# Performance work log

Measured on AMD Instinct MI355X. Metric: run time of the kernel, lower is better.

Reference implementation:

```python
import math
import jax, jax.numpy as jnp
import numpy as np

B, T, C = 2, 2048, 1024
H = 16
HD = C // H
WIN = 33
HALF = WIN // 2
CAUSAL = True
RADIUS, OMEGA, KSPR, STEP = 6.0, 1.0, 1.0, 0.1
EPS = 1e-8


def _spiral_step(x):
    # x: (..., 3) — the stacked (q, k, v) axis; D=3 -> rotate (x0, x1) pair.
    r = jnp.maximum(jnp.linalg.norm(x, axis=-1, keepdims=True), EPS)
    radial = (RADIUS - r) * (x / r)
    c = jnp.float32(math.cos(OMEGA * STEP))
    s = jnp.float32(math.sin(OMEGA * STEP))
    xi, xj, xl = x[..., 0], x[..., 1], x[..., 2]
    y = jnp.stack([c * xi - s * xj, s * xi + c * xj, xl], axis=-1)
    return x + STEP * (y - x + KSPR * radial)


def setup_inputs() -> dict:
    key = jax.random.key(0)
    ks = jax.random.split(key, 3)
    x = jax.random.normal(ks[0], (B, T, C), dtype=jnp.float32)
    W_attn = jax.random.normal(ks[1], (C, 3 * C), dtype=jnp.float32) * (1.0 / math.sqrt(C))
    W_proj = jax.random.normal(ks[2], (C, C), dtype=jnp.float32) * (1.0 / math.sqrt(C))
    sinks = jnp.zeros((H,), dtype=jnp.float32)
    ln_scale = jnp.ones((1,), dtype=jnp.float32) * 0.9
    ln_delta = jnp.ones((C,), dtype=jnp.float32)
    ln_bias = jnp.zeros((C,), dtype=jnp.float32)
    return {"x": x, "W_attn": W_attn, "W_proj": W_proj, "sinks": sinks,
            "ln_scale": ln_scale, "ln_delta": ln_delta, "ln_bias": ln_bias}


def reference(x, W_attn, W_proj, sinks, ln_scale, ln_delta, ln_bias):
    qkv = x @ W_attn                              # (B,T,3C)
    q, k, v = jnp.split(qkv, 3, axis=-1)          # each (B,T,C)

    # SpiralMix over the stacked (q,k,v) axis, loop_iters=2. Only q,k are
    # taken from the mixed output (v stays the pre-spiral value), matching src.
    s = jnp.stack([q, k, v], axis=-1)             # (B,T,C,3)
    s = _spiral_step(_spiral_step(s))
    q, k = s[..., 0], s[..., 1]

    def to_heads(t):
        return t.reshape(B, T, H, HD).transpose(0, 2, 1, 3)  # (B,H,T,hd)
    q, k, v = to_heads(q), to_heads(k), to_heads(v)

    # local window index
    t_idx = jnp.arange(T)
    offs = jnp.arange(-HALF, HALF + 1)
    neigh = t_idx[:, None] + offs[None, :]                    # (T,W)
    valid = (neigh >= 0) & (neigh < T)
    if CAUSAL:
        valid &= neigh <= t_idx[:, None]
    neigh_c = jnp.clip(neigh, 0, T - 1)

    k_n = k[:, :, neigh_c, :]                                 # (B,H,T,W,hd)
    v_n = v[:, :, neigh_c, :]

    inv_sqrt_d = 1.0 / math.sqrt(HD)
    scores = jnp.einsum('bhtd,bhtwd->bhtw',
                        q.astype(jnp.float32), k_n.astype(jnp.float32)) * inv_sqrt_d
    scores = jnp.where(valid[None, None], scores, -jnp.inf)

    # softmax with learned sink logits per head
    sinks_b = sinks.reshape(1, H, 1, 1).astype(scores.dtype)
    m = jnp.max(scores, axis=-1, keepdims=True)
    mj = jnp.maximum(m, sinks_b)
    exp_s = jnp.exp(scores - mj)
    denom = jnp.sum(exp_s, axis=-1, keepdims=True) + jnp.exp(sinks_b - mj)
    att = exp_s / denom                                       # (B,H,T,W)

    y = jnp.einsum('bhtw,bhtwd->bhtd', att, v_n.astype(att.dtype))
    y = y.transpose(0, 2, 1, 3).reshape(B, T, C).astype(x.dtype)
    y = y @ W_proj
    y = jnp.tanh(ln_scale * y)
    return ln_delta * y + ln_bias
```

## Files before the change

### kernel.cpp

```cpp
#include <hip/hip_runtime.h>
#include <hip/hip_fp16.h>
#include <math.h>

#define T_DIM 2048
#define B_DIM 2
#define C_DIM 1024
#define H_DIM 16
#define M_DIM 4096

typedef _Float16 f16x8 __attribute__((ext_vector_type(8)));
typedef _Float16 f16x4 __attribute__((ext_vector_type(4)));
typedef _Float16 f16x2 __attribute__((ext_vector_type(2)));
typedef float    f32x4 __attribute__((ext_vector_type(4)));

union f16x8_u { f16x8 v; f16x2 h[4]; _Float16 e[8]; };

#if defined(__has_builtin)
#  if __has_builtin(__builtin_amdgcn_fdot2)
#    define HAVE_FDOT2 1
#  endif
#endif

static __device__ __forceinline__ float FDOT2(f16x2 a, f16x2 b, float c)
{
#ifdef HAVE_FDOT2
    return __builtin_amdgcn_fdot2(a, b, c, false);
#else
    return c + (float)a[0] * (float)b[0] + (float)a[1] * (float)b[1];
#endif
}

#define ASYNC_COPY16(gsrc, ldst) \
  __builtin_amdgcn_global_load_lds( \
    (__attribute__((address_space(1))) unsigned int*)(gsrc), \
    (__attribute__((address_space(3))) unsigned int*)(ldst), 16, 0, 0)

__global__ __launch_bounds__(256) void prep_kernel(const float* __restrict__ x,
                                                   const float* __restrict__ Wa,
                                                   const float* __restrict__ Wp,
                                                   _Float16* __restrict__ xh,
                                                   _Float16* __restrict__ WaT,
                                                   _Float16* __restrict__ WpT)
{
    __shared__ float tile[32][33];
    const int bid = blockIdx.x;
    const int tid = threadIdx.x;
    if (bid < 4096) {
        const int i = bid * 256 + tid;
        float4 v = ((const float4*)x)[i];
        f16x4 o;
        o[0] = (_Float16)v.x; o[1] = (_Float16)v.y;
        o[2] = (_Float16)v.z; o[3] = (_Float16)v.w;
        ((f16x4*)xh)[i] = o;
        return;
    }
    const float* W; _Float16* WT; int N, b;
    if (bid < 4096 + 3072) { W = Wa; WT = WaT; N = 3072; b = bid - 4096; }
    else                   { W = Wp; WT = WpT; N = 1024; b = bid - 7168; }
    const int K = 1024;
    const int bk = b & 31;
    const int bn = b >> 5;
    const int tx = tid & 31, ty = tid >> 5;
#pragma unroll
    for (int r = ty; r < 32; r += 8)
        tile[r][tx] = W[(long)(bk * 32 + r) * N + bn * 32 + tx];
    __syncthreads();
#pragma unroll
    for (int r = ty; r < 32; r += 8)
        WT[(long)(bn * 32 + r) * K + bk * 32 + tx] = (_Float16)tile[tx][r];
}

template<int BM, int EPI, int OUTF16>
__global__ __launch_bounds__(256) void gemm_f16_kernel(
    const _Float16* __restrict__ A, const _Float16* __restrict__ Bt,
    void* __restrict__ Cv, int M, int N, int K,
    const float* __restrict__ ln_scale, const float* __restrict__ ln_delta,
    const float* __restrict__ ln_bias)
{
    constexpr int M_REP   = BM / 32;
    constexpr int A_LOADS = BM / 64;
    constexpr int LPT     = A_LOADS + 2;
    __shared__ __attribute__((aligned(16))) _Float16 As[3][BM * 32];
    __shared__ __attribute__((aligned(16))) _Float16 Bs[3][128 * 32];

    const int tid  = threadIdx.x;
    const int lane = tid & 63;
    const int wave = tid >> 6;
    const int wr = wave >> 1, wc = wave & 1;

    const int nwg = gridDim.x;
    const int q8  = nwg >> 3;
    const int bid = ((int)blockIdx.x & 7) * q8 + ((int)blockIdx.x >> 3);

    const int ntn = N >> 7;
    const int m0 = (bid / ntn) * BM;
    const int n0 = (bid % ntn) << 7;

    f32x4 acc[M_REP][4] = {};

    const int ea   = tid * 8;
    const int erow = ea >> 5;
    const int xm   = ((erow & 2) << 3) | ((erow & 4) << 1);
    const int ecs  = (ea & 31) ^ xm;
    const _Float16* aptr[A_LOADS];
    const _Float16* bptr[2];
#pragma unroll
    for (int l = 0; l < A_LOADS; ++l)
        aptr[l] = A + (long)(m0 + erow + l * 64) * K + ecs;
#pragma unroll
    for (int l = 0; l < 2; ++l)
        bptr[l] = Bt + (long)(n0 + erow + l * 64) * K + ecs;

    const int fr = lane & 15;
    const int kb = (lane >> 4) << 3;
    const int xr = ((fr & 2) << 3) | ((fr & 4) << 1);
    const int kbs = kb ^ xr;
    const int NT = K >> 5;

    auto stage = [&](int tile, int slot) {
        const int k0 = tile << 5;
#pragma unroll
        for (int l = 0; l < A_LOADS; ++l) ASYNC_COPY16(aptr[l] + k0, &As[slot][ea + l * 2048]);
#pragma unroll
        for (int l = 0; l < 2; ++l)       ASYNC_COPY16(bptr[l] + k0, &Bs[slot][ea + l * 2048]);
    };

    stage(0, 0);
    stage(1, 1);

    int s = 0;
    for (int t = 0; t < NT; ++t) {
        if (t + 2 < NT) {
            int s2 = s + 2; if (s2 >= 3) s2 -= 3;
            stage(t + 2, s2);
        }
        const int rem = NT - 1 - t;
        if constexpr (LPT == 4) {
            if (rem >= 2)      asm volatile("s_waitcnt vmcnt(8)" ::: "memory");
            else if (rem == 1) asm volatile("s_waitcnt vmcnt(4)" ::: "memory");
            else               asm volatile("s_waitcnt vmcnt(0)" ::: "memory");
        } else {
            if (rem >= 2)      asm volatile("s_waitcnt vmcnt(6)" ::: "memory");
            else if (rem == 1) asm volatile("s_waitcnt vmcnt(3)" ::: "memory");
            else               asm volatile("s_waitcnt vmcnt(0)" ::: "memory");
        }
        __syncthreads();

        f16x8 af[M_REP], bf[4];
#pragma unroll
        for (int i = 0; i < M_REP; i++)
            af[i] = *(const f16x8*)&As[s][((wr * (BM / 2) + (i << 4) + fr) << 5) + kbs];
#pragma unroll
        for (int j = 0; j < 4; j++)
            bf[j] = *(const f16x8*)&Bs[s][(((wc << 6) + (j << 4) + fr) << 5) + kbs];
        __builtin_amdgcn_s_setprio(1);
#pragma unroll
        for (int i = 0; i < M_REP; i++)
#pragma unroll
            for (int j = 0; j < 4; j++)
                acc[i][j] = __builtin_amdgcn_mfma_f32_16x16x32_f16(af[i], bf[j], acc[i][j], 0, 0, 0);
        __builtin_amdgcn_s_setprio(0);
        if (t + 1 < NT) __syncthreads();
        ++s; if (s == 3) s = 0;
    }

    const int rsub = (lane >> 4) << 2;
    const float lsc = EPI ? ln_scale[0] : 0.f;
#pragma unroll
    for (int j = 0; j < 4; j++) {
        const int col = n0 + (wc << 6) + (j << 4) + fr;
        float ld = 0.f, lb = 0.f;
        if (EPI) { ld = ln_delta[col]; lb = ln_bias[col]; }
#pragma unroll
        for (int i = 0; i < M_REP; i++) {
            const int rbase = m0 + wr * (BM / 2) + (i << 4) + rsub;
#pragma unroll
            for (int r = 0; r < 4; r++) {
                float v = acc[i][j][r];
                if (EPI) v = ld * tanhf(lsc * v) + lb;
                if (OUTF16) ((_Float16*)Cv)[(long)(rbase + r) * N + col] = (_Float16)v;
                else        ((float*)Cv)[(long)(rbase + r) * N + col] = v;
            }
        }
    }
}

__device__ __forceinline__ void spiral2(float& xi, float& xj, float xl)
{
    const float CS = 0.9950041652780258f;
    const float SN = 0.09983341664682815f;
#pragma unroll
    for (int s = 0; s < 2; s++) {
        float r = sqrtf(xi * xi + xj * xj + xl * xl);
        r = fmaxf(r, 1e-8f);
        const float coef = (6.0f - r) / r;
        const float yi = CS * xi - SN * xj;
        const float yj = SN * xi + CS * xj;
        const float nxi = xi + 0.1f * (yi - xi + coef * xi);
        const float nxj = xj + 0.1f * (yj - xj + coef * xj);
        const float nxl = xl + 0.1f * (coef * xl);
        xi = nxi; xj = nxj; xl = nxl;
    }
}

#define TB   128
#define ROWS 144
#define LDR  72

__global__ __launch_bounds__(128) void attn_kernel(const _Float16* __restrict__ qkv,
                                                   const float* __restrict__ sinks,
                                                   _Float16* __restrict__ yh)
{
    __shared__ __attribute__((aligned(16))) _Float16 k_lds[ROWS * LDR];
    __shared__ __attribute__((aligned(16))) _Float16 v_lds[ROWS * LDR];
    __shared__ __attribute__((aligned(16))) _Float16 q_lds[TB * LDR];

    const int tid = threadIdx.x;
    const int chunk = blockIdx.x & 15;
    const int h = (blockIdx.x >> 4) & 15;
    const int b = blockIdx.x >> 8;
    const int t0 = chunk * TB;
    const long bT = (long)b * T_DIM;

    for (int s = tid; s < ROWS * 4; s += 128) {
        const int ri = s >> 2, q4 = s & 3;
        const int gr = min(max(t0 - 16 + ri, 0), T_DIM - 1);
        const _Float16* base = qkv + (bT + gr) * 3072 + (h << 6) + (q4 << 4);
        f16x8_u qa, qb, ka, kb2, va, vb;
        qa.v  = *(const f16x8*)(base);        qb.v  = *(const f16x8*)(base + 8);
        ka.v  = *(const f16x8*)(base + 1024); kb2.v = *(const f16x8*)(base + 1032);
        va.v  = *(const f16x8*)(base + 2048); vb.v  = *(const f16x8*)(base + 2056);
        float qq[16], kk[16], vv[16];
#pragma unroll
        for (int u = 0; u < 8; u++) {
            qq[u] = (float)qa.e[u]; qq[8 + u] = (float)qb.e[u];
            kk[u] = (float)ka.e[u]; kk[8 + u] = (float)kb2.e[u];
            vv[u] = (float)va.e[u]; vv[8 + u] = (float)vb.e[u];
        }
#pragma unroll
        for (int u = 0; u < 16; u++) spiral2(qq[u], kk[u], vv[u]);
        const int lbase = ri * LDR + (q4 << 4);
        f16x8_u ko0, ko1, vo0, vo1;
#pragma unroll
        for (int u = 0; u < 8; u++) {
            ko0.e[u] = (_Float16)kk[u]; ko1.e[u] = (_Float16)kk[8 + u];
            vo0.e[u] = (_Float16)vv[u]; vo1.e[u] = (_Float16)vv[8 + u];
        }
        *(f16x8*)&k_lds[lbase]     = ko0.v;
        *(f16x8*)&k_lds[lbase + 8] = ko1.v;
        *(f16x8*)&v_lds[lbase]     = vo0.v;
        *(f16x8*)&v_lds[lbase + 8] = vo1.v;
        if (ri >= 16) {
            const int qbase = (ri - 16) * LDR + (q4 << 4);
            f16x8_u qo0, qo1;
#pragma unroll
            for (int u = 0; u < 8; u++) {
                qo0.e[u] = (_Float16)(qq[u] * 0.125f);
                qo1.e[u] = (_Float16)(qq[8 + u] * 0.125f);
            }
            *(f16x8*)&q_lds[qbase]     = qo0.v;
            *(f16x8*)&q_lds[qbase + 8] = qo1.v;
        }
    }
    __syncthreads();

    f16x8_u qv[8];
#pragma unroll
    for (int u = 0; u < 8; u++) qv[u].v = *(const f16x8*)&q_lds[tid * LDR + u * 8];

    float sc[17];
#pragma unroll
    for (int j = 0; j < 17; j++) {
        const _Float16* kr = &k_lds[(tid + j) * LDR];
        float s = 0.f;
#pragma unroll
        for (int u = 0; u < 8; u++) {
            f16x8_u kx; kx.v = *(const f16x8*)&kr[u * 8];
#pragma unroll
            for (int p = 0; p < 4; p++) s = FDOT2(qv[u].h[p], kx.h[p], s);
        }
        sc[j] = s;
    }

    const int t = t0 + tid;
#pragma unroll
    for (int j = 0; j < 17; j++)
        if (j + t < 16) sc[j] = -INFINITY;
    const float sink = sinks[h];
    float m = sink;
#pragma unroll
    for (int j = 0; j < 17; j++) m = fmaxf(m, sc[j]);
    float e[17];
    float denom = expf(sink - m);
#pragma unroll
    for (int j = 0; j < 17; j++) { e[j] = expf(sc[j] - m); denom += e[j]; }
    const float rden = 1.f / denom;
#pragma unroll
    for (int j = 0; j < 17; j++) e[j] *= rden;

    float yacc[64];
#pragma unroll
    for (int d = 0; d < 64; d++) yacc[d] = 0.f;
#pragma unroll
    for (int j = 0; j < 17; j++) {
        const float a = e[j];
        const _Float16* vr = &v_lds[(tid + j) * LDR];
#pragma unroll
        for (int u = 0; u < 8; u++) {
            f16x8_u vx; vx.v = *(const f16x8*)&vr[u * 8];
#pragma unroll
            for (int z = 0; z < 8; z++) yacc[u * 8 + z] += a * (float)vx.e[z];
        }
    }

#pragma unroll
    for (int u = 0; u < 8; u++) {
        f16x8_u yo;
#pragma unroll
        for (int z = 0; z < 8; z++) yo.e[z] = (_Float16)yacc[u * 8 + z];
        *(f16x8*)&q_lds[tid * LDR + u * 8] = yo.v;
    }
    __syncthreads();
    const int ch = tid & 7, rb = tid >> 3;
#pragma unroll
    for (int pass = 0; pass < 8; ++pass) {
        const int r = pass * 16 + rb;
        *(f16x8*)(yh + (bT + t0 + r) * 1024 + (h << 6) + ch * 8) =
            *(const f16x8*)&q_lds[r * LDR + ch * 8];
    }
}

extern "C" void kernel_launch(void* const* d_in, const int* in_sizes, int n_in,
                              void* d_out, int out_size, void* d_ws, size_t ws_size,
                              hipStream_t stream)
{
    const float* x        = (const float*)d_in[0];
    const float* W_attn   = (const float*)d_in[1];
    const float* W_proj   = (const float*)d_in[2];
    const float* sinks    = (const float*)d_in[3];
    const float* ln_scale = (const float*)d_in[4];
    const float* ln_delta = (const float*)d_in[5];
    const float* ln_bias  = (const float*)d_in[6];
    float* out = (float*)d_out;

    char* ws = (char*)d_ws;
    _Float16* xh    = (_Float16*)(ws);
    _Float16* WaT   = (_Float16*)(ws + (size_t)( 8u << 20));
    _Float16* WpT   = (_Float16*)(ws + (size_t)(14u << 20));
    _Float16* qkv16 = (_Float16*)(ws + (size_t)(16u << 20));
    _Float16* yh    = (_Float16*)(ws + (size_t)(40u << 20));

    prep_kernel<<<8192, 256, 0, stream>>>(x, W_attn, W_proj, xh, WaT, WpT);
    gemm_f16_kernel<128, 0, 1><<<32 * 24, 256, 0, stream>>>(xh, WaT, qkv16, 4096, 3072, 1024,
                                                            nullptr, nullptr, nullptr);
    attn_kernel<<<512, 128, 0, stream>>>(qkv16, sinks, yh);
    gemm_f16_kernel<64, 1, 0><<<64 * 8, 256, 0, stream>>>(yh, WpT, out, 4096, 1024, 1024,
                                                          ln_scale, ln_delta, ln_bias);
}
```

Baseline: 172.6 us.

## Pre-pack QKV GEMM operands into MFMA fragment layout and stream without LDS

Splits the prep kernel into three kernels. Two of them write x and W_attn in a packed per-lane MFMA fragment order, so the QKV GEMM can load fragments straight from global memory into registers without LDS staging, async copies or barriers. Each wave computes a 64x64 tile independently. This removes LDS traffic and synchronisation but gives up shared-memory reuse between waves, which adds global and L2 traffic, and it adds two extra kernel launches.

```diff
diff --git a/kernel.cpp b/kernel.cpp
--- a/kernel.cpp
+++ b/kernel.cpp
@@ -35,45 +35,123 @@
     (__attribute__((address_space(1))) unsigned int*)(gsrc), \
     (__attribute__((address_space(3))) unsigned int*)(ldst), 16, 0, 0)
 
-__global__ __launch_bounds__(256) void prep_kernel(const float* __restrict__ x,
-                                                   const float* __restrict__ Wa,
-                                                   const float* __restrict__ Wp,
-                                                   _Float16* __restrict__ xh,
-                                                   _Float16* __restrict__ WaT,
-                                                   _Float16* __restrict__ WpT)
-{
-    __shared__ float tile[32][33];
-    const int bid = blockIdx.x;
+
+__global__ __launch_bounds__(256) void prep_xpack_kernel(const float* __restrict__ x,
+                                                         _Float16* __restrict__ xpack)
+{
+    __shared__ __attribute__((aligned(16))) _Float16 rows[16 * 1032];
+    const int g = blockIdx.x;
     const int tid = threadIdx.x;
-    if (bid < 4096) {
-        const int i = bid * 256 + tid;
-        float4 v = ((const float4*)x)[i];
+    const int row = tid >> 4, c16 = tid & 15;
+#pragma unroll
+    for (int it = 0; it < 16; ++it) {
+        const int c4 = (c16 + it * 16) << 2;
+        float4 v = *(const float4*)&x[(long)(g * 16 + row) * 1024 + c4];
         f16x4 o;
         o[0] = (_Float16)v.x; o[1] = (_Float16)v.y;
         o[2] = (_Float16)v.z; o[3] = (_Float16)v.w;
-        ((f16x4*)xh)[i] = o;
-        return;
-    }
-    const float* W; _Float16* WT; int N, b;
-    if (bid < 4096 + 3072) { W = Wa; WT = WaT; N = 3072; b = bid - 4096; }
-    else                   { W = Wp; WT = WpT; N = 1024; b = bid - 7168; }
-    const int K = 1024;
+        *(f16x4*)&rows[row * 1032 + c4] = o;
+    }
+    __syncthreads();
+    const int l = tid & 63, ksb = tid >> 6;
+#pragma unroll
+    for (int cc = 0; cc < 8; ++cc) {
+        const int ks = ksb + cc * 4;
+        f16x8 c = *(const f16x8*)&rows[(l & 15) * 1032 + ks * 32 + ((l >> 4) << 3)];
+        *(f16x8*)&xpack[((long)(g * 32 + ks)) * 512 + l * 8] = c;
+    }
+}
+
+__global__ __launch_bounds__(256) void prep_wapack_kernel(const float* __restrict__ W,
+                                                          _Float16* __restrict__ wpack)
+{
+    __shared__ float tile[32][33];
+    const int b = blockIdx.x;
     const int bk = b & 31;
     const int bn = b >> 5;
+    const int tid = threadIdx.x;
     const int tx = tid & 31, ty = tid >> 5;
+    const int N = 3072;
 #pragma unroll
     for (int r = ty; r < 32; r += 8)
         tile[r][tx] = W[(long)(bk * 32 + r) * N + bn * 32 + tx];
     __syncthreads();
+    if (tid < 128) {
+        const int hh = tid >> 6, l = tid & 63;
+        const int kb = (l >> 4) << 3;
+        f16x8_u o;
+#pragma unroll
+        for (int j = 0; j < 8; ++j)
+            o.e[j] = (_Float16)tile[kb + j][hh * 16 + (l & 15)];
+        *(f16x8*)&wpack[((long)((bn * 2 + hh) * 32 + bk)) * 512 + l * 8] = o.v;
+    }
+}
+
+__global__ __launch_bounds__(256) void prep_wpt_kernel(const float* __restrict__ W,
+                                                       _Float16* __restrict__ WT)
+{
+    __shared__ float tile[32][33];
+    const int N = 1024, K = 1024;
+    const int bk = blockIdx.x & 31;
+    const int bn = blockIdx.x >> 5;
+    const int tx = threadIdx.x & 31, ty = threadIdx.x >> 5;
+#pragma unroll
+    for (int r = ty; r < 32; r += 8)
+        tile[r][tx] = W[(long)(bk * 32 + r) * N + bn * 32 + tx];
+    __syncthreads();
 #pragma unroll
     for (int r = ty; r < 32; r += 8)
         WT[(long)(bn * 32 + r) * K + bk * 32 + tx] = (_Float16)tile[tx][r];
 }
 
-template<int BM, int EPI, int OUTF16>
-__global__ __launch_bounds__(256) void gemm_f16_kernel(
+__global__ __launch_bounds__(256) void gemm1_stream_kernel(const _Float16* __restrict__ Apack,
+                                                           const _Float16* __restrict__ Bpack,
+                                                           _Float16* __restrict__ C)
+{
+    const int lane = threadIdx.x & 63;
+    const int wid  = threadIdx.x >> 6;
+    const int bid = ((int)blockIdx.x & 7) * 96 + ((int)blockIdx.x >> 3);
+    const int mw = bid & 63;
+    const int nw = (bid >> 6) * 4 + wid;
+
+    const _Float16* abase = Apack + ((long)(mw * 4) * 32) * 512 + lane * 8;
+    const _Float16* bbase = Bpack + ((long)(nw * 4) * 32) * 512 + lane * 8;
+
+    f32x4 acc[4][4] = {};
+
+#pragma unroll 2
+    for (int t = 0; t < 32; ++t) {
+        f16x8 af[4], bf[4];
+#pragma unroll
+        for (int i = 0; i < 4; i++) af[i] = *(const f16x8*)(abase + (i * 32 + t) * 512);
+#pragma unroll
+        for (int j = 0; j < 4; j++) bf[j] = *(const f16x8*)(bbase + (j * 32 + t) * 512);
+#pragma unroll
+        for (int i = 0; i < 4; i++)
+#pragma unroll
+            for (int j = 0; j < 4; j++)
+                acc[i][j] = __builtin_amdgcn_mfma_f32_16x16x32_f16(af[i], bf[j], acc[i][j], 0, 0, 0);
+    }
+
+    const int fr = lane & 15;
+    const int rsub = (lane >> 4) << 2;
+#pragma unroll
+    for (int j = 0; j < 4; j++) {
+        const int col = nw * 64 + j * 16 + fr;
+#pragma unroll
+        for (int i = 0; i < 4; i++) {
+            const int rbase = mw * 64 + i * 16 + rsub;
+#pragma unroll
+            for (int r = 0; r < 4; r++)
+                C[(long)(rbase + r) * 3072 + col] = (_Float16)acc[i][j][r];
+        }
+    }
+}
+
+template<int BM>
+__global__ __launch_bounds__(256) void gemm2_kernel(
     const _Float16* __restrict__ A, const _Float16* __restrict__ Bt,
-    void* __restrict__ Cv, int M, int N, int K,
+    float* __restrict__ Cv, int M, int N, int K,
     const float* __restrict__ ln_scale, const float* __restrict__ ln_delta,
     const float* __restrict__ ln_bias)
 {
@@ -135,15 +213,9 @@
             stage(t + 2, s2);
         }
         const int rem = NT - 1 - t;
-        if constexpr (LPT == 4) {
-            if (rem >= 2)      asm volatile("s_waitcnt vmcnt(8)" ::: "memory");
-            else if (rem == 1) asm volatile("s_waitcnt vmcnt(4)" ::: "memory");
-            else               asm volatile("s_waitcnt vmcnt(0)" ::: "memory");
-        } else {
-            if (rem >= 2)      asm volatile("s_waitcnt vmcnt(6)" ::: "memory");
-            else if (rem == 1) asm volatile("s_waitcnt vmcnt(3)" ::: "memory");
-            else               asm volatile("s_waitcnt vmcnt(0)" ::: "memory");
-        }
+        if (rem >= 2)      asm volatile("s_waitcnt vmcnt(6)" ::: "memory");
+        else if (rem == 1) asm volatile("s_waitcnt vmcnt(3)" ::: "memory");
+        else               asm volatile("s_waitcnt vmcnt(0)" ::: "memory");
         __syncthreads();
 
         f16x8 af[M_REP], bf[4];
@@ -165,21 +237,19 @@
     }
 
     const int rsub = (lane >> 4) << 2;
-    const float lsc = EPI ? ln_scale[0] : 0.f;
+    const float lsc = ln_scale[0];
 #pragma unroll
     for (int j = 0; j < 4; j++) {
         const int col = n0 + (wc << 6) + (j << 4) + fr;
-        float ld = 0.f, lb = 0.f;
-        if (EPI) { ld = ln_delta[col]; lb = ln_bias[col]; }
+        const float ld = ln_delta[col], lb = ln_bias[col];
 #pragma unroll
         for (int i = 0; i < M_REP; i++) {
             const int rbase = m0 + wr * (BM / 2) + (i << 4) + rsub;
 #pragma unroll
             for (int r = 0; r < 4; r++) {
                 float v = acc[i][j][r];
-                if (EPI) v = ld * tanhf(lsc * v) + lb;
-                if (OUTF16) ((_Float16*)Cv)[(long)(rbase + r) * N + col] = (_Float16)v;
-                else        ((float*)Cv)[(long)(rbase + r) * N + col] = v;
+                v = ld * tanhf(lsc * v) + lb;
+                Cv[(long)(rbase + r) * N + col] = v;
             }
         }
     }
@@ -344,16 +414,17 @@
     float* out = (float*)d_out;
 
     char* ws = (char*)d_ws;
-    _Float16* xh    = (_Float16*)(ws);
-    _Float16* WaT   = (_Float16*)(ws + (size_t)( 8u << 20));
-    _Float16* WpT   = (_Float16*)(ws + (size_t)(14u << 20));
-    _Float16* qkv16 = (_Float16*)(ws + (size_t)(16u << 20));
-    _Float16* yh    = (_Float16*)(ws + (size_t)(40u << 20));
-
-    prep_kernel<<<8192, 256, 0, stream>>>(x, W_attn, W_proj, xh, WaT, WpT);
-    gemm_f16_kernel<128, 0, 1><<<32 * 24, 256, 0, stream>>>(xh, WaT, qkv16, 4096, 3072, 1024,
-                                                            nullptr, nullptr, nullptr);
+    _Float16* xpack  = (_Float16*)(ws);
+    _Float16* wapack = (_Float16*)(ws + (size_t)( 8u << 20));
+    _Float16* WpT    = (_Float16*)(ws + (size_t)(14u << 20));
+    _Float16* qkv16  = (_Float16*)(ws + (size_t)(16u << 20));
+    _Float16* yh     = (_Float16*)(ws + (size_t)(40u << 20));
+
+    prep_xpack_kernel <<<256,  256, 0, stream>>>(x, xpack);
+    prep_wapack_kernel<<<3072, 256, 0, stream>>>(W_attn, wapack);
+    prep_wpt_kernel   <<<1024, 256, 0, stream>>>(W_proj, WpT);
+    gemm1_stream_kernel<<<768, 256, 0, stream>>>(xpack, wapack, qkv16);
     attn_kernel<<<512, 128, 0, stream>>>(qkv16, sinks, yh);
-    gemm_f16_kernel<64, 1, 0><<<64 * 8, 256, 0, stream>>>(yh, WpT, out, 4096, 1024, 1024,
-                                                          ln_scale, ln_delta, ln_bias);
-}
+    gemm2_kernel<64><<<64 * 8, 256, 0, stream>>>(yh, WpT, out, 4096, 1024, 1024,
+                                                 ln_scale, ln_delta, ln_bias);
+}
```

Result: slower. 178.2 us (+3.2%).
